# Kernel optimization log

Measured on AMD Instinct MI355X. Metric: run time of the kernel, lower is better.

Reference implementation:

```python
import jax, jax.numpy as jnp
import numpy as np

BS, S, H, KVH, HD = 4, 4096, 32, 8, 128
BLK = 32                      # tokens per cache page
NB = S // BLK                 # blocks per sequence (128)
NPAGES = BS * NB              # total pages in pool (512)
WIN = 1024                    # sliding window
G = H // KVH                  # query heads per KV head (GQA group)
SCALE = 1.0 / float(np.sqrt(HD))
NEG = -1e30


def setup_inputs() -> dict:
    key = jax.random.key(0)
    k0, k1, k2, k3 = jax.random.split(key, 4)
    q = jax.random.normal(k0, (BS, S, H, HD), dtype=jnp.float32)
    k = jax.random.normal(k1, (BS, S, KVH, HD), dtype=jnp.float32)
    v = jax.random.normal(k2, (BS, S, KVH, HD), dtype=jnp.float32)
    k_cache = jnp.zeros((NPAGES, BLK, KVH, HD), dtype=jnp.float32)
    v_cache = jnp.zeros((NPAGES, BLK, KVH, HD), dtype=jnp.float32)
    # identity block table: page p holds block (p % NB) of sequence (p // NB)
    seq_block_ids = jnp.arange(NPAGES, dtype=jnp.int32).reshape(BS, NB)
    start_positions = jnp.full((BS,), S - 1, dtype=jnp.int32)  # decode last token
    mask = jnp.zeros((BS, 1, 1, S), dtype=jnp.float32)         # additive mask
    sink = jax.random.normal(k3, (H,), dtype=jnp.float32)      # per-head sink logit
    return {"q": q, "k": k, "v": v, "k_cache": k_cache, "v_cache": v_cache,
            "mask": mask, "sink": sink, "seq_block_ids": seq_block_ids,
            "start_positions": start_positions}


def reference(q, k, v, k_cache, v_cache, mask, sink, seq_block_ids, start_positions):
    # ---- prefill: write full k/v into the paged cache ----
    # (the wrapper discards the prefill attention output; cache write is its
    #  only observable effect on the returned decode output)
    kp = k.reshape(BS, NB, BLK, KVH, HD)
    vp = v.reshape(BS, NB, BLK, KVH, HD)
    k_cache = k_cache.at[seq_block_ids].set(kp)
    v_cache = v_cache.at[seq_block_ids].set(vp)

    # ---- decode: write last-token k/v at start_positions ----
    b = jnp.arange(BS)
    pages = seq_block_ids[b, start_positions // BLK]   # [BS]
    offs = start_positions % BLK                       # [BS]
    k_cache = k_cache.at[pages, offs].set(k[:, -1])
    v_cache = v_cache.at[pages, offs].set(v[:, -1])

    # ---- gather cache back into dense [BS, S, KVH, HD] via block table ----
    k_all = k_cache[seq_block_ids].reshape(BS, S, KVH, HD)
    v_all = v_cache[seq_block_ids].reshape(BS, S, KVH, HD)

    # ---- last-token paged attention with sliding window + sink ----
    q_last = q[:, -1].reshape(BS, KVH, G, HD)          # group query heads by KV head
    scores = jnp.einsum('bhgd,bjhd->bhgj', q_last, k_all) * SCALE  # [BS,KVH,G,S]
    scores = scores + mask                              # mask broadcasts over heads
    pos = jnp.arange(S, dtype=jnp.int32)
    p = start_positions[:, None]
    valid = (pos[None, :] <= p) & (p - pos[None, :] < WIN)          # [BS,S]
    scores = jnp.where(valid[:, None, None, :], scores, NEG)

    # softmax with an extra per-head sink logit that contributes no value
    sink_l = sink.reshape(KVH, G)[None, :, :, None]     # [1,KVH,G,1]
    m = jnp.maximum(jnp.max(scores, axis=-1, keepdims=True), sink_l)
    e = jnp.exp(scores - m)
    denom = jnp.sum(e, axis=-1, keepdims=True) + jnp.exp(sink_l - m)
    attn = e / denom                                    # [BS,KVH,G,S]

    out = jnp.einsum('bhgj,bjhd->bhgd', attn, v_all)    # [BS,KVH,G,HD]
    return out.reshape(BS, 1, H, HD)
```

## Files before the change

### kernel.cpp

```cpp
#include <hip/hip_runtime.h>
#include <math.h>

#define BS 4
#define S 4096
#define H 32
#define KVH 8
#define HD 128
#define G 4
#define WIN 1024
#define SCALE 0.08838834764831843f

#define NSPLIT 32
#define CHUNK (WIN / NSPLIT)
#define PSTRIDE 132

#define GLOAD_LDS16(gsrc, ldst) \
    __builtin_amdgcn_global_load_lds( \
        (const __attribute__((address_space(1))) void*)(gsrc), \
        (__attribute__((address_space(3))) void*)(ldst), 16, 0, 0)

#define READLANE_F(x, l) \
    __uint_as_float(__builtin_amdgcn_readlane(__float_as_uint(x), (l)))

template <int CTRL>
__device__ __forceinline__ float dpp_mov(float x) {
    return __int_as_float(__builtin_amdgcn_update_dpp(
        0, __float_as_int(x), CTRL, 0xF, 0xF, true));
}
__device__ __forceinline__ float red_add16(float d) {
    d += dpp_mov<0xB1>(d);
    d += dpp_mov<0x4E>(d);
    d += dpp_mov<0x124>(d);
    d += dpp_mov<0x128>(d);
    return d;
}
__device__ __forceinline__ float red_max16(float d) {
    d = fmaxf(d, dpp_mov<0xB1>(d));
    d = fmaxf(d, dpp_mov<0x4E>(d));
    d = fmaxf(d, dpp_mov<0x124>(d));
    d = fmaxf(d, dpp_mov<0x128>(d));
    return d;
}

__global__ __launch_bounds__(256) void attn_split_kernel(
    const float* __restrict__ q, const float* __restrict__ k,
    const float* __restrict__ v, const float* __restrict__ mask,
    const int* __restrict__ start_positions, float* __restrict__ ws)
{
    const int blk   = blockIdx.x;
    const int split = blk % NSPLIT;
    const int kvh   = (blk / NSPLIT) % KVH;
    const int b     = blk / (NSPLIT * KVH);
    const int tid   = threadIdx.x;
    const int g     = tid >> 6;
    const int lane  = tid & 63;
    const int grp   = lane >> 4;
    const int l16   = lane & 15;
    const int h     = kvh * G + g;

    const int p = start_positions[b];
    const int base_pos = p - WIN + 1 + split * CHUNK;

    __shared__ float kbuf[CHUNK][HD];
    __shared__ float sc[G][CHUNK];

    const size_t kv_base = (size_t)b * S * (KVH * HD) + (size_t)kvh * HD;
    const int srow = lane >> 5;
    const int scol = (lane & 31) * 4;

    #pragma unroll
    for (int i = 0; i < 4; ++i) {
        const int st  = g * 4 + i;
        const int r   = st * 2 + srow;
        const int pos = base_pos + r;
        const int row = (pos == p) ? (S - 1) : (pos < 0 ? 0 : pos);
        GLOAD_LDS16(k + kv_base + (size_t)row * (KVH * HD) + scol,
                    (char*)&kbuf[0][0] + st * 1024);
    }

    const int lpos = base_pos + (lane & 31);
    const float msk = (lpos >= 0) ? mask[(size_t)b * S + lpos] : 0.f;

    const float* qptr = q + (((size_t)b * S + (S - 1)) * H + h) * HD + l16 * 8;
    const float4 qa = *(const float4*)(qptr);
    const float4 qb = *(const float4*)(qptr + 4);

    __syncthreads();

    const int half = lane >> 5;
    const int l32  = lane & 31;
    float4 vreg[CHUNK / 2];
    #pragma unroll
    for (int it = 0; it < CHUNK / 2; ++it) {
        const int jj  = it * 2 + half;
        const int pos = base_pos + jj;
        const int row = (pos == p) ? (S - 1) : (pos < 0 ? 0 : pos);
        vreg[it] = *(const float4*)(v + kv_base + (size_t)row * (KVH * HD) + l32 * 4);
    }
    asm volatile("" ::: "memory");

    #pragma unroll
    for (int it = 0; it < CHUNK / 4; ++it) {
        const int jj = it * 4 + grp;
        const float4 ka = *(const float4*)(&kbuf[jj][l16 * 8]);
        const float4 kb = *(const float4*)(&kbuf[jj][l16 * 8 + 4]);
        float d = qa.x * ka.x + qa.y * ka.y + qa.z * ka.z + qa.w * ka.w
                + qb.x * kb.x + qb.y * kb.y + qb.z * kb.z + qb.w * kb.w;
        d = red_add16(d);
        if (l16 == 0) sc[g][jj] = d;
    }

    float s_l = sc[g][lane & (CHUNK - 1)] * SCALE + msk;
    if (lpos < 0) s_l = -1e30f;
    float m = red_max16(s_l);
    m = fmaxf(m, __shfl_xor(m, 16, 64));
    const float e_l = __expf(s_l - m);
    float lsum = red_add16(e_l);
    lsum += __shfl_xor(lsum, 16, 64);

    float4 o4 = make_float4(0.f, 0.f, 0.f, 0.f);
    #pragma unroll
    for (int it = 0; it < CHUNK / 2; ++it) {
        const float e0 = READLANE_F(e_l, it * 2);
        const float e1 = READLANE_F(e_l, it * 2 + 1);
        const float e  = half ? e1 : e0;
        o4.x += e * vreg[it].x; o4.y += e * vreg[it].y;
        o4.z += e * vreg[it].z; o4.w += e * vreg[it].w;
    }
    o4.x += __shfl_xor(o4.x, 32, 64);
    o4.y += __shfl_xor(o4.y, 32, 64);
    o4.z += __shfl_xor(o4.z, 32, 64);
    o4.w += __shfl_xor(o4.w, 32, 64);

    const size_t widx = ((((size_t)b * KVH + kvh) * G + g) * NSPLIT + split) * (size_t)PSTRIDE;
    if (lane < 32) {
        *(float4*)(ws + widx + 4 * l32) = o4;
        if (lane == 0) {
            float2 ml; ml.x = m; ml.y = lsum;
            *(float2*)(ws + widx + 128) = ml;
        }
    }
}

__global__ __launch_bounds__(256) void attn_reduce_kernel(
    const float* __restrict__ ws, const float* __restrict__ sink,
    float* __restrict__ out)
{
    const int blk = blockIdx.x;
    const int h = blk % H;
    const int b = blk / H;
    const int kvh = h / G;
    const int g = h % G;
    const int tid = threadIdx.x;
    const int w = tid >> 6;
    const int lane = tid & 63;

    const size_t base = ((((size_t)b * KVH + kvh) * G + g) * (size_t)NSPLIT) * (size_t)PSTRIDE;

    __shared__ float red_m[4];
    __shared__ float red_d[4];
    __shared__ float red_o[4][HD];

    const float sk = sink[h];

    float2 ml[8];
    float Mw = -1e30f;
    #pragma unroll
    for (int i = 0; i < 8; ++i) {
        ml[i] = *(const float2*)(ws + base + (size_t)(w * 8 + i) * PSTRIDE + 128);
        Mw = fmaxf(Mw, ml[i].x);
    }
    if (lane == 0) red_m[w] = Mw;
    __syncthreads();
    float M = fmaxf(fmaxf(red_m[0], red_m[1]), fmaxf(red_m[2], red_m[3]));
    M = fmaxf(M, sk);

    float D = 0.f, ax = 0.f, ay = 0.f;
    #pragma unroll
    for (int i = 0; i < 8; ++i) {
        const size_t rec = base + (size_t)(w * 8 + i) * PSTRIDE;
        const float wgt = __expf(ml[i].x - M);
        D += wgt * ml[i].y;
        const float2 o2 = *(const float2*)(ws + rec + 2 * lane);
        ax += wgt * o2.x;
        ay += wgt * o2.y;
    }
    if (lane == 0) red_d[w] = D;
    red_o[w][2 * lane]     = ax;
    red_o[w][2 * lane + 1] = ay;
    __syncthreads();

    if (w == 0) {
        const float Dt = red_d[0] + red_d[1] + red_d[2] + red_d[3] + __expf(sk - M);
        const float ox = red_o[0][2 * lane] + red_o[1][2 * lane]
                       + red_o[2][2 * lane] + red_o[3][2 * lane];
        const float oy = red_o[0][2 * lane + 1] + red_o[1][2 * lane + 1]
                       + red_o[2][2 * lane + 1] + red_o[3][2 * lane + 1];
        const float invD = 1.f / Dt;
        float2 r; r.x = ox * invD; r.y = oy * invD;
        *(float2*)(out + ((size_t)b * H + h) * HD + 2 * lane) = r;
    }
}

extern "C" void kernel_launch(void* const* d_in, const int* in_sizes, int n_in,
                              void* d_out, int out_size, void* d_ws, size_t ws_size,
                              hipStream_t stream) {
    const float* q    = (const float*)d_in[0];
    const float* k    = (const float*)d_in[1];
    const float* v    = (const float*)d_in[2];
    const float* mask = (const float*)d_in[5];
    const float* sink = (const float*)d_in[6];
    const int* start_positions = (const int*)d_in[8];
    float* out = (float*)d_out;
    float* ws  = (float*)d_ws;

    attn_split_kernel<<<BS * KVH * NSPLIT, 256, 0, stream>>>(q, k, v, mask, start_positions, ws);
    attn_reduce_kernel<<<BS * H, 256, 0, stream>>>(ws, sink, out);
}
```

Measured before the change: 14.50 us.

## Halve split count and double-buffer K staging over two sub-chunks per block

Each split block now covers 64 keys instead of 32, processed as two 32-key sub-chunks. The second K sub-chunk is staged into a separate LDS buffer while the first is being consumed, and the two partial softmax results are merged online inside the block. This halves the split-kernel grid and the number of partial records the reduce kernel reads, cutting per-block overhead and reduce traffic. In exchange there are fewer blocks for latency hiding, longer per-block serial work, extra register pressure from the second V register set, and an added barrier.

```diff
diff --git a/kernel.cpp b/kernel.cpp
--- a/kernel.cpp
+++ b/kernel.cpp
@@ -10,8 +10,9 @@
 #define WIN 1024
 #define SCALE 0.08838834764831843f
 
-#define NSPLIT 32
-#define CHUNK (WIN / NSPLIT)
+#define NSPLIT 16
+#define CHUNK 64
+#define SUB 32
 #define PSTRIDE 132
 
 #define GLOAD_LDS16(gsrc, ldst) \
@@ -57,29 +58,37 @@
     const int grp   = lane >> 4;
     const int l16   = lane & 15;
     const int h     = kvh * G + g;
+    const int half  = lane >> 5;
+    const int l32   = lane & 31;
 
     const int p = start_positions[b];
     const int base_pos = p - WIN + 1 + split * CHUNK;
 
-    __shared__ float kbuf[CHUNK][HD];
-    __shared__ float sc[G][CHUNK];
+    __shared__ float kbuf[2][SUB][HD];
+    __shared__ float sc[G][SUB];
 
     const size_t kv_base = (size_t)b * S * (KVH * HD) + (size_t)kvh * HD;
     const int srow = lane >> 5;
     const int scol = (lane & 31) * 4;
 
-    #pragma unroll
-    for (int i = 0; i < 4; ++i) {
-        const int st  = g * 4 + i;
-        const int r   = st * 2 + srow;
-        const int pos = base_pos + r;
-        const int row = (pos == p) ? (S - 1) : (pos < 0 ? 0 : pos);
-        GLOAD_LDS16(k + kv_base + (size_t)row * (KVH * HD) + scol,
-                    (char*)&kbuf[0][0] + st * 1024);
-    }
-
-    const int lpos = base_pos + (lane & 31);
-    const float msk = (lpos >= 0) ? mask[(size_t)b * S + lpos] : 0.f;
+    auto stageK = [&](int buf, int sub_base) {
+        #pragma unroll
+        for (int i = 0; i < 4; ++i) {
+            const int st  = g * 4 + i;
+            const int r   = st * 2 + srow;
+            const int pos = sub_base + r;
+            const int row = (pos == p) ? (S - 1) : (pos < 0 ? 0 : pos);
+            GLOAD_LDS16(k + kv_base + (size_t)row * (KVH * HD) + scol,
+                        (char*)&kbuf[buf][0][0] + st * 1024);
+        }
+    };
+
+    stageK(0, base_pos);
+
+    const int lpos0 = base_pos + l32;
+    const int lpos1 = base_pos + SUB + l32;
+    const float msk0 = (lpos0 >= 0) ? mask[(size_t)b * S + lpos0] : 0.f;
+    const float msk1 = (lpos1 >= 0) ? mask[(size_t)b * S + lpos1] : 0.f;
 
     const float* qptr = q + (((size_t)b * S + (S - 1)) * H + h) * HD + l16 * 8;
     const float4 qa = *(const float4*)(qptr);
@@ -87,46 +96,96 @@
 
     __syncthreads();
 
-    const int half = lane >> 5;
-    const int l32  = lane & 31;
-    float4 vreg[CHUNK / 2];
-    #pragma unroll
-    for (int it = 0; it < CHUNK / 2; ++it) {
-        const int jj  = it * 2 + half;
-        const int pos = base_pos + jj;
+    stageK(1, base_pos + SUB);
+
+    float4 v0[SUB / 2];
+    #pragma unroll
+    for (int it = 0; it < SUB / 2; ++it) {
+        const int pos = base_pos + it * 2 + half;
         const int row = (pos == p) ? (S - 1) : (pos < 0 ? 0 : pos);
-        vreg[it] = *(const float4*)(v + kv_base + (size_t)row * (KVH * HD) + l32 * 4);
+        v0[it] = *(const float4*)(v + kv_base + (size_t)row * (KVH * HD) + l32 * 4);
     }
     asm volatile("" ::: "memory");
 
     #pragma unroll
-    for (int it = 0; it < CHUNK / 4; ++it) {
+    for (int it = 0; it < SUB / 4; ++it) {
         const int jj = it * 4 + grp;
-        const float4 ka = *(const float4*)(&kbuf[jj][l16 * 8]);
-        const float4 kb = *(const float4*)(&kbuf[jj][l16 * 8 + 4]);
+        const float4 ka = *(const float4*)(&kbuf[0][jj][l16 * 8]);
+        const float4 kb = *(const float4*)(&kbuf[0][jj][l16 * 8 + 4]);
         float d = qa.x * ka.x + qa.y * ka.y + qa.z * ka.z + qa.w * ka.w
                 + qb.x * kb.x + qb.y * kb.y + qb.z * kb.z + qb.w * kb.w;
         d = red_add16(d);
         if (l16 == 0) sc[g][jj] = d;
     }
 
-    float s_l = sc[g][lane & (CHUNK - 1)] * SCALE + msk;
-    if (lpos < 0) s_l = -1e30f;
-    float m = red_max16(s_l);
-    m = fmaxf(m, __shfl_xor(m, 16, 64));
-    const float e_l = __expf(s_l - m);
-    float lsum = red_add16(e_l);
-    lsum += __shfl_xor(lsum, 16, 64);
-
-    float4 o4 = make_float4(0.f, 0.f, 0.f, 0.f);
-    #pragma unroll
-    for (int it = 0; it < CHUNK / 2; ++it) {
-        const float e0 = READLANE_F(e_l, it * 2);
-        const float e1 = READLANE_F(e_l, it * 2 + 1);
-        const float e  = half ? e1 : e0;
-        o4.x += e * vreg[it].x; o4.y += e * vreg[it].y;
-        o4.z += e * vreg[it].z; o4.w += e * vreg[it].w;
-    }
+    float s0 = sc[g][l32] * SCALE + msk0;
+    if (lpos0 < 0) s0 = -1e30f;
+    float m0 = red_max16(s0);
+    m0 = fmaxf(m0, __shfl_xor(m0, 16, 64));
+    const float e0 = __expf(s0 - m0);
+    float l0 = red_add16(e0);
+    l0 += __shfl_xor(l0, 16, 64);
+
+    float4 oa = make_float4(0.f, 0.f, 0.f, 0.f);
+    #pragma unroll
+    for (int it = 0; it < SUB / 2; ++it) {
+        const float ea = READLANE_F(e0, it * 2);
+        const float eb = READLANE_F(e0, it * 2 + 1);
+        const float e  = half ? eb : ea;
+        oa.x += e * v0[it].x; oa.y += e * v0[it].y;
+        oa.z += e * v0[it].z; oa.w += e * v0[it].w;
+    }
+
+    __syncthreads();
+
+    float4 v1[SUB / 2];
+    #pragma unroll
+    for (int it = 0; it < SUB / 2; ++it) {
+        const int pos = base_pos + SUB + it * 2 + half;
+        const int row = (pos == p) ? (S - 1) : (pos < 0 ? 0 : pos);
+        v1[it] = *(const float4*)(v + kv_base + (size_t)row * (KVH * HD) + l32 * 4);
+    }
+    asm volatile("" ::: "memory");
+
+    #pragma unroll
+    for (int it = 0; it < SUB / 4; ++it) {
+        const int jj = it * 4 + grp;
+        const float4 ka = *(const float4*)(&kbuf[1][jj][l16 * 8]);
+        const float4 kb = *(const float4*)(&kbuf[1][jj][l16 * 8 + 4]);
+        float d = qa.x * ka.x + qa.y * ka.y + qa.z * ka.z + qa.w * ka.w
+                + qb.x * kb.x + qb.y * kb.y + qb.z * kb.z + qb.w * kb.w;
+        d = red_add16(d);
+        if (l16 == 0) sc[g][jj] = d;
+    }
+
+    float s1 = sc[g][l32] * SCALE + msk1;
+    if (lpos1 < 0) s1 = -1e30f;
+    float m1 = red_max16(s1);
+    m1 = fmaxf(m1, __shfl_xor(m1, 16, 64));
+    const float e1 = __expf(s1 - m1);
+    float l1 = red_add16(e1);
+    l1 += __shfl_xor(l1, 16, 64);
+
+    float4 ob = make_float4(0.f, 0.f, 0.f, 0.f);
+    #pragma unroll
+    for (int it = 0; it < SUB / 2; ++it) {
+        const float ea = READLANE_F(e1, it * 2);
+        const float eb = READLANE_F(e1, it * 2 + 1);
+        const float e  = half ? eb : ea;
+        ob.x += e * v1[it].x; ob.y += e * v1[it].y;
+        ob.z += e * v1[it].z; ob.w += e * v1[it].w;
+    }
+
+    const float mm = fmaxf(m0, m1);
+    const float w0 = __expf(m0 - mm);
+    const float w1 = __expf(m1 - mm);
+    const float lsum = l0 * w0 + l1 * w1;
+    float4 o4;
+    o4.x = oa.x * w0 + ob.x * w1;
+    o4.y = oa.y * w0 + ob.y * w1;
+    o4.z = oa.z * w0 + ob.z * w1;
+    o4.w = oa.w * w0 + ob.w * w1;
+
     o4.x += __shfl_xor(o4.x, 32, 64);
     o4.y += __shfl_xor(o4.y, 32, 64);
     o4.z += __shfl_xor(o4.z, 32, 64);
@@ -136,8 +195,8 @@
     if (lane < 32) {
         *(float4*)(ws + widx + 4 * l32) = o4;
         if (lane == 0) {
-            float2 ml; ml.x = m; ml.y = lsum;
-            *(float2*)(ws + widx + 128) = ml;
+            float2 ml2; ml2.x = mm; ml2.y = lsum;
+            *(float2*)(ws + widx + 128) = ml2;
         }
     }
 }
@@ -163,11 +222,11 @@
 
     const float sk = sink[h];
 
-    float2 ml[8];
+    float2 ml[4];
     float Mw = -1e30f;
     #pragma unroll
-    for (int i = 0; i < 8; ++i) {
-        ml[i] = *(const float2*)(ws + base + (size_t)(w * 8 + i) * PSTRIDE + 128);
+    for (int i = 0; i < 4; ++i) {
+        ml[i] = *(const float2*)(ws + base + (size_t)(w * 4 + i) * PSTRIDE + 128);
         Mw = fmaxf(Mw, ml[i].x);
     }
     if (lane == 0) red_m[w] = Mw;
@@ -177,8 +236,8 @@
 
     float D = 0.f, ax = 0.f, ay = 0.f;
     #pragma unroll
-    for (int i = 0; i < 8; ++i) {
-        const size_t rec = base + (size_t)(w * 8 + i) * PSTRIDE;
+    for (int i = 0; i < 4; ++i) {
+        const size_t rec = base + (size_t)(w * 4 + i) * PSTRIDE;
         const float wgt = __expf(ml[i].x - M);
         D += wgt * ml[i].y;
         const float2 o2 = *(const float2*)(ws + rec + 2 * lane);
```

Result: slower. 14.88 us (+2.6%).

## Split attention into one-wave blocks per query head, dropping LDS K staging

Applied to the files above, without the earlier changes.

The split kernel now launches one 64-thread wave per (batch, kv head, split, query head) instead of a 256-thread block shared by the four GQA heads. K rows are read straight from global memory into registers, replacing the LDS staging via global_load_lds and the block-wide barrier. V loads are split into two halves, with the second half issued after the QK dot products to cut register pressure and overlap loads with compute. The cost is that each K/V chunk is now fetched by four separate waves, relying on cache hits instead of shared LDS reuse.

```diff
diff --git a/kernel.cpp b/kernel.cpp
--- a/kernel.cpp
+++ b/kernel.cpp
@@ -14,11 +14,6 @@
 #define CHUNK (WIN / NSPLIT)
 #define PSTRIDE 132
 
-#define GLOAD_LDS16(gsrc, ldst) \
-    __builtin_amdgcn_global_load_lds( \
-        (const __attribute__((address_space(1))) void*)(gsrc), \
-        (__attribute__((address_space(3))) void*)(ldst), 16, 0, 0)
-
 #define READLANE_F(x, l) \
     __uint_as_float(__builtin_amdgcn_readlane(__float_as_uint(x), (l)))
 
@@ -42,75 +37,70 @@
     return d;
 }
 
-__global__ __launch_bounds__(256) void attn_split_kernel(
+__global__ __launch_bounds__(64) void attn_split_kernel(
     const float* __restrict__ q, const float* __restrict__ k,
     const float* __restrict__ v, const float* __restrict__ mask,
     const int* __restrict__ start_positions, float* __restrict__ ws)
 {
     const int blk   = blockIdx.x;
-    const int split = blk % NSPLIT;
-    const int kvh   = (blk / NSPLIT) % KVH;
-    const int b     = blk / (NSPLIT * KVH);
-    const int tid   = threadIdx.x;
-    const int g     = tid >> 6;
-    const int lane  = tid & 63;
+    const int g     = blk & (G - 1);
+    const int split = (blk >> 2) & (NSPLIT - 1);
+    const int kvh   = (blk >> 7) & (KVH - 1);
+    const int b     = blk >> 10;
+    const int lane  = threadIdx.x;
     const int grp   = lane >> 4;
     const int l16   = lane & 15;
+    const int half  = lane >> 5;
+    const int l32   = lane & 31;
     const int h     = kvh * G + g;
 
     const int p = start_positions[b];
     const int base_pos = p - WIN + 1 + split * CHUNK;
 
-    __shared__ float kbuf[CHUNK][HD];
-    __shared__ float sc[G][CHUNK];
+    __shared__ float sc[CHUNK];
 
     const size_t kv_base = (size_t)b * S * (KVH * HD) + (size_t)kvh * HD;
-    const int srow = lane >> 5;
-    const int scol = (lane & 31) * 4;
-
-    #pragma unroll
-    for (int i = 0; i < 4; ++i) {
-        const int st  = g * 4 + i;
-        const int r   = st * 2 + srow;
-        const int pos = base_pos + r;
-        const int row = (pos == p) ? (S - 1) : (pos < 0 ? 0 : pos);
-        GLOAD_LDS16(k + kv_base + (size_t)row * (KVH * HD) + scol,
-                    (char*)&kbuf[0][0] + st * 1024);
-    }
-
-    const int lpos = base_pos + (lane & 31);
+
+    const int lpos = base_pos + l32;
     const float msk = (lpos >= 0) ? mask[(size_t)b * S + lpos] : 0.f;
 
     const float* qptr = q + (((size_t)b * S + (S - 1)) * H + h) * HD + l16 * 8;
     const float4 qa = *(const float4*)(qptr);
     const float4 qb = *(const float4*)(qptr + 4);
 
-    __syncthreads();
-
-    const int half = lane >> 5;
-    const int l32  = lane & 31;
-    float4 vreg[CHUNK / 2];
-    #pragma unroll
-    for (int it = 0; it < CHUNK / 2; ++it) {
-        const int jj  = it * 2 + half;
+    float4 va[CHUNK / 4];
+    #pragma unroll
+    for (int it = 0; it < CHUNK / 4; ++it) {
+        const int pos = base_pos + it * 2 + half;
+        const int row = (pos == p) ? (S - 1) : (pos < 0 ? 0 : pos);
+        va[it] = *(const float4*)(v + kv_base + (size_t)row * (KVH * HD) + l32 * 4);
+    }
+    asm volatile("" ::: "memory");
+
+    #pragma unroll
+    for (int it = 0; it < CHUNK / 4; ++it) {
+        const int jj  = it * 4 + grp;
         const int pos = base_pos + jj;
         const int row = (pos == p) ? (S - 1) : (pos < 0 ? 0 : pos);
-        vreg[it] = *(const float4*)(v + kv_base + (size_t)row * (KVH * HD) + l32 * 4);
-    }
-    asm volatile("" ::: "memory");
-
-    #pragma unroll
-    for (int it = 0; it < CHUNK / 4; ++it) {
-        const int jj = it * 4 + grp;
-        const float4 ka = *(const float4*)(&kbuf[jj][l16 * 8]);
-        const float4 kb = *(const float4*)(&kbuf[jj][l16 * 8 + 4]);
+        const float* kp = k + kv_base + (size_t)row * (KVH * HD) + l16 * 8;
+        const float4 ka = *(const float4*)(kp);
+        const float4 kb = *(const float4*)(kp + 4);
         float d = qa.x * ka.x + qa.y * ka.y + qa.z * ka.z + qa.w * ka.w
                 + qb.x * kb.x + qb.y * kb.y + qb.z * kb.z + qb.w * kb.w;
         d = red_add16(d);
-        if (l16 == 0) sc[g][jj] = d;
-    }
-
-    float s_l = sc[g][lane & (CHUNK - 1)] * SCALE + msk;
+        if (l16 == 0) sc[jj] = d;
+    }
+
+    float4 vb[CHUNK / 4];
+    #pragma unroll
+    for (int it = 0; it < CHUNK / 4; ++it) {
+        const int pos = base_pos + 16 + it * 2 + half;
+        const int row = (pos == p) ? (S - 1) : (pos < 0 ? 0 : pos);
+        vb[it] = *(const float4*)(v + kv_base + (size_t)row * (KVH * HD) + l32 * 4);
+    }
+    asm volatile("" ::: "memory");
+
+    float s_l = sc[l32] * SCALE + msk;
     if (lpos < 0) s_l = -1e30f;
     float m = red_max16(s_l);
     m = fmaxf(m, __shfl_xor(m, 16, 64));
@@ -120,12 +110,20 @@
 
     float4 o4 = make_float4(0.f, 0.f, 0.f, 0.f);
     #pragma unroll
-    for (int it = 0; it < CHUNK / 2; ++it) {
+    for (int it = 0; it < CHUNK / 4; ++it) {
         const float e0 = READLANE_F(e_l, it * 2);
         const float e1 = READLANE_F(e_l, it * 2 + 1);
         const float e  = half ? e1 : e0;
-        o4.x += e * vreg[it].x; o4.y += e * vreg[it].y;
-        o4.z += e * vreg[it].z; o4.w += e * vreg[it].w;
+        o4.x += e * va[it].x; o4.y += e * va[it].y;
+        o4.z += e * va[it].z; o4.w += e * va[it].w;
+    }
+    #pragma unroll
+    for (int it = 0; it < CHUNK / 4; ++it) {
+        const float e0 = READLANE_F(e_l, 16 + it * 2);
+        const float e1 = READLANE_F(e_l, 16 + it * 2 + 1);
+        const float e  = half ? e1 : e0;
+        o4.x += e * vb[it].x; o4.y += e * vb[it].y;
+        o4.z += e * vb[it].z; o4.w += e * vb[it].w;
     }
     o4.x += __shfl_xor(o4.x, 32, 64);
     o4.y += __shfl_xor(o4.y, 32, 64);
@@ -214,6 +212,7 @@
     float* out = (float*)d_out;
     float* ws  = (float*)d_ws;
 
-    attn_split_kernel<<<BS * KVH * NSPLIT, 256, 0, stream>>>(q, k, v, mask, start_positions, ws);
+    attn_split_kernel<<<BS * KVH * NSPLIT * G, 64, 0, stream>>>(
+        q, k, v, mask, start_positions, ws);
     attn_reduce_kernel<<<BS * H, 256, 0, stream>>>(ws, sink, out);
 }
```

New measurement: 27.33 us. 88.4% more time.
